# Performance work log

Measured on AMD Instinct MI355X. Metric: run time of the kernel, lower is better.

Reference implementation:

```python
import jax, jax.numpy as jnp
import numpy as np

N, C, H, W = 4, 64, 64, 64
K = 3


def _unfold(x, k):
    """torch F.unfold with padding k//2: [n,c,h,w] -> [n, c*k*k, h*w].
    Feature ordering matches torch: index = c*k*k + i*k + j."""
    p = k // 2
    n, c, h, w = x.shape
    xp = jnp.pad(x, ((0, 0), (0, 0), (p, p), (p, p)))
    patches = jnp.stack(
        [xp[:, :, i:i + h, j:j + w] for i in range(k) for j in range(k)], axis=2
    )  # [n, c, k*k, h, w]
    return patches.reshape(n, c * k * k, h * w)


def _mask_vec(c, k):
    # causal patch mask from __init__: zero out center-and-right of middle row and all rows below
    m = np.ones((c, k, k), np.float32)
    m[:, k // 2, k // 2:] = 0
    m[:, k // 2 + 1:, :] = 0
    return jnp.asarray(m.reshape(1, c * k * k, 1))


def setup_inputs() -> dict:
    key = jax.random.key(0)
    k1, k2 = jax.random.split(key)
    y_hat = jax.random.normal(k1, (N, C, H, W), dtype=jnp.float32)
    y_prob = jax.random.uniform(k2, (N, 1, H, W), dtype=jnp.float32)
    return {"y_hat": y_hat, "y_prob": y_prob}


def reference(y_hat, y_prob):
    k = K
    n, c, h, w = y_hat.shape
    L = h * w
    mask = _mask_vec(c, k)

    u = _unfold(y_hat, k) * mask                              # [n, c*k*k, L]
    u = u / jnp.maximum(jnp.linalg.norm(u, axis=1, keepdims=True), 1e-12)
    R = jnp.einsum('nfl,nfm->nlm', u, u)                      # [n, L, L] cosine sims

    # eval path: keep strictly-upper triangle (causal: l < m)
    row = jnp.arange(L)[:, None]
    col = jnp.arange(L)[None, :]
    R = jnp.where(col > row, R, 0.0)

    R_star = jnp.max(R, axis=1)                               # [n, L]
    arg = jnp.argmax(R, axis=1).astype(jnp.int32)             # [n, L]

    y_unf = _unfold(y_hat, k)                                 # [n, c*k*k, L]
    ref_unfold = jnp.take_along_axis(y_unf, arg[:, None, :], axis=2)

    prob_unf = y_prob.reshape(n, -1, L)                       # 1x1 unfold
    U_unf = jnp.take_along_axis(prob_unf, arg[:, None, :], axis=2)

    S = R_star.reshape(n, 1, h, w)
    U = U_unf.reshape(n, -1, h, w)

    # eval-mode position-0 overrides
    S = S.at[:, :, 0, 0].set(1e-8)
    U = U.at[:, :, 0, 0].set(1e-8)
    ref_unfold = ref_unfold.at[:, :, 0].set(0.0)
    arg = arg.at[:, 0].set(-1)

    S = jnp.clip(S, 1e-8, 1.0)
    U = jnp.clip(U, 1e-8, 1.0)
    return S, U, ref_unfold, arg
```

## Files before the change

### kernel.cpp

```cpp
#include <hip/hip_runtime.h>
#include <stdint.h>

#define Nn 4
#define Cc 64
#define LL 4096
#define KK 256
#define TRI2 528

typedef _Float16 half8 __attribute__((ext_vector_type(8)));
typedef float f32x16 __attribute__((ext_vector_type(16)));
typedef float f32x4 __attribute__((ext_vector_type(4)));
typedef unsigned short ushort8v __attribute__((ext_vector_type(8)));

__device__ __forceinline__ unsigned f2ord(float f) {
    unsigned u = __float_as_uint(f);
    return u ^ ((u & 0x80000000u) ? 0xFFFFFFFFu : 0x80000000u);
}
__device__ __forceinline__ float ord2f(unsigned o) {
    unsigned u = (o & 0x80000000u) ? (o ^ 0x80000000u) : ~o;
    return __uint_as_float(u);
}
__device__ __forceinline__ unsigned short h2u(_Float16 h) {
    union { _Float16 f; unsigned short u; } x; x.f = h; return x.u;
}

__global__ __launch_bounds__(256) void build_v(const float* __restrict__ yhat,
                                               unsigned short* __restrict__ VhT,
                                               unsigned short* __restrict__ VlT,
                                               float* __restrict__ yhatT,
                                               unsigned long long* __restrict__ best) {
    int blk = blockIdx.x;
    int xcd = blk & 7;
    int n = xcd >> 1;
    int i64 = (blk >> 3) + (xcd & 1) * 128;
    int tid = threadIdx.x;
    if (tid < 16) best[(size_t)n * LL + i64 * 16 + tid] = 0ull;

    int cg = tid & 15;
    int l = i64 * 16 + (tid >> 4);
    int y = l >> 6, x = l & 63;
    const float* src = yhat + (size_t)n * (Cc * LL);

    float vals[16];
    float ctr[4];
    float sumsq = 0.f;
#pragma unroll
    for (int ci = 0; ci < 4; ++ci) {
        const float* p = src + (cg * 4 + ci) * LL;
        float t0 = (y > 0 && x > 0)  ? p[l - 65] : 0.f;
        float t1 = (y > 0)           ? p[l - 64] : 0.f;
        float t2 = (y > 0 && x < 63) ? p[l - 63] : 0.f;
        float t3 = (x > 0)           ? p[l - 1]  : 0.f;
        ctr[ci] = p[l];
        vals[ci * 4 + 0] = t0; vals[ci * 4 + 1] = t1;
        vals[ci * 4 + 2] = t2; vals[ci * 4 + 3] = t3;
        sumsq += t0 * t0 + t1 * t1 + t2 * t2 + t3 * t3;
    }
    sumsq += __shfl_xor(sumsq, 1, 64);
    sumsq += __shfl_xor(sumsq, 2, 64);
    sumsq += __shfl_xor(sumsq, 4, 64);
    sumsq += __shfl_xor(sumsq, 8, 64);
    float inv = 1.f / fmaxf(sqrtf(sumsq), 1e-12f);

    f32x4 cv; cv.x = ctr[0]; cv.y = ctr[1]; cv.z = ctr[2]; cv.w = ctr[3];
    *(f32x4*)(yhatT + ((size_t)n * LL + l) * 64 + cg * 4) = cv;

    size_t pk = ((((size_t)n * 128 + (l >> 5)) * 16 + cg) << 9) + (l & 31) * 8;
    unsigned short* dh = VhT + pk;
    unsigned short* dl = VlT + pk;
    ushort8v hA, hB, lA, lB;
#pragma unroll
    for (int kk = 0; kk < 16; ++kk) {
        float v = vals[kk] * inv;
        _Float16 h = (fabsf(v) < 6.1035e-5f) ? (_Float16)0 : (_Float16)v;
        _Float16 lo = (_Float16)((v - (float)h) * 2048.0f);
        unsigned short hu = h2u(h * (_Float16)2048.0f);
        unsigned short lu = h2u(lo);
        if (kk < 8) { hA[kk] = hu; lA[kk] = lu; }
        else        { hB[kk - 8] = hu; lB[kk - 8] = lu; }
    }
    *(ushort8v*)(dh)       = hA;
    *(ushort8v*)(dh + 256) = hB;
    *(ushort8v*)(dl)       = lA;
    *(ushort8v*)(dl + 256) = lB;
}

__device__ __forceinline__ void loadset(const unsigned short* Ah0, const unsigned short* Ah1,
                                        const unsigned short* Al0, const unsigned short* Al1,
                                        const unsigned short* Bh0, const unsigned short* Bh1,
                                        const unsigned short* Bl0, const unsigned short* Bl1,
                                        int le,
                                        half8 (&al)[2][2], half8 (&ah)[2][2],
                                        half8 (&bl)[2][2], half8 (&bh)[2][2]) {
    al[0][0] = *(const half8*)(Al0 + le);       al[0][1] = *(const half8*)(Al0 + 512 + le);
    al[1][0] = *(const half8*)(Al1 + le);       al[1][1] = *(const half8*)(Al1 + 512 + le);
    bh[0][0] = *(const half8*)(Bh0 + le);       bh[0][1] = *(const half8*)(Bh0 + 512 + le);
    bh[1][0] = *(const half8*)(Bh1 + le);       bh[1][1] = *(const half8*)(Bh1 + 512 + le);
    ah[0][0] = *(const half8*)(Ah0 + le);       ah[0][1] = *(const half8*)(Ah0 + 512 + le);
    ah[1][0] = *(const half8*)(Ah1 + le);       ah[1][1] = *(const half8*)(Ah1 + 512 + le);
    bl[0][0] = *(const half8*)(Bl0 + le);       bl[0][1] = *(const half8*)(Bl0 + 512 + le);
    bl[1][0] = *(const half8*)(Bl1 + le);       bl[1][1] = *(const half8*)(Bl1 + 512 + le);
}

__device__ __forceinline__ void mfmaset(half8 (&al)[2][2], half8 (&ah)[2][2],
                                        half8 (&bl)[2][2], half8 (&bh)[2][2],
                                        f32x16 (&acc)[2][2]) {
    __builtin_amdgcn_s_setprio(1);
#pragma unroll
    for (int kc = 0; kc < 2; ++kc)
#pragma unroll
        for (int r = 0; r < 2; ++r)
#pragma unroll
            for (int c = 0; c < 2; ++c)
                acc[r][c] = __builtin_amdgcn_mfma_f32_32x32x16_f16(al[r][kc], bh[c][kc], acc[r][c], 0, 0, 0);
#pragma unroll
    for (int kc = 0; kc < 2; ++kc)
#pragma unroll
        for (int r = 0; r < 2; ++r)
#pragma unroll
            for (int c = 0; c < 2; ++c)
                acc[r][c] = __builtin_amdgcn_mfma_f32_32x32x16_f16(ah[r][kc], bl[c][kc], acc[r][c], 0, 0, 0);
#pragma unroll
    for (int kc = 0; kc < 2; ++kc)
#pragma unroll
        for (int r = 0; r < 2; ++r)
#pragma unroll
            for (int c = 0; c < 2; ++c)
                acc[r][c] = __builtin_amdgcn_mfma_f32_32x32x16_f16(ah[r][kc], bh[c][kc], acc[r][c], 0, 0, 0);
    __builtin_amdgcn_s_setprio(0);
}

__global__ __launch_bounds__(256) void simmax(const unsigned short* __restrict__ Vh,
                                              const unsigned short* __restrict__ Vl,
                                              unsigned long long* __restrict__ best) {
    int bx = blockIdx.x;
    int xcd = bx & 7, idx = bx >> 3;
    int n = xcd >> 1;
    int t = (xcd & 1) * 264 + idx;
    int j = (int)((sqrtf(8.f * (float)t + 1.f) - 1.f) * 0.5f);
    while ((j + 1) * (j + 2) / 2 <= t) ++j;
    while (j * (j + 1) / 2 > t) --j;
    int i = t - j * (j + 1) / 2;
    int l0 = i * 128, m0 = j * 128;

    int tid = threadIdx.x;
    int w = tid >> 6, lane = tid & 63;
    int r5 = lane & 31, h5 = lane >> 5;
    int rw = (w & 1) * 64;
    int cw = (w >> 1) * 64;
    if ((i == j) && (rw == 64) && (cw == 0)) return;

    const unsigned short* VhB = Vh + (size_t)n * (LL * KK);
    const unsigned short* VlB = Vl + (size_t)n * (LL * KK);

    int aRow = __builtin_amdgcn_readfirstlane((l0 + rw) >> 5);
    int bRow = __builtin_amdgcn_readfirstlane((m0 + cw) >> 5);
    const unsigned short* Ah0 = VhB + ((size_t)aRow << 13);
    const unsigned short* Ah1 = Ah0 + 8192;
    const unsigned short* Al0 = VlB + ((size_t)aRow << 13);
    const unsigned short* Al1 = Al0 + 8192;
    const unsigned short* Bh0 = VhB + ((size_t)bRow << 13);
    const unsigned short* Bh1 = Bh0 + 8192;
    const unsigned short* Bl0 = VlB + ((size_t)bRow << 13);
    const unsigned short* Bl1 = Bl0 + 8192;
    int le = lane * 8;

    f32x16 acc[2][2];
#pragma unroll
    for (int r = 0; r < 2; ++r)
#pragma unroll
        for (int c = 0; c < 2; ++c) acc[r][c] = (f32x16)0.f;

    half8 alA[2][2], ahA[2][2], blA[2][2], bhA[2][2];
    half8 alB[2][2], ahB[2][2], blB[2][2], bhB[2][2];

#define BUMP() do { Ah0 += 1024; Ah1 += 1024; Al0 += 1024; Al1 += 1024; \
                    Bh0 += 1024; Bh1 += 1024; Bl0 += 1024; Bl1 += 1024; } while (0)

    loadset(Ah0, Ah1, Al0, Al1, Bh0, Bh1, Bl0, Bl1, le, alA, ahA, blA, bhA);
    BUMP();
#pragma unroll 1
    for (int it = 0; it < 4; ++it) {
        loadset(Ah0, Ah1, Al0, Al1, Bh0, Bh1, Bl0, Bl1, le, alB, ahB, blB, bhB);
        BUMP();
        mfmaset(alA, ahA, blA, bhA, acc);
        if (it < 3) {
            loadset(Ah0, Ah1, Al0, Al1, Bh0, Bh1, Bl0, Bl1, le, alA, ahA, blA, bhA);
            BUMP();
        }
        mfmaset(alB, ahB, blB, bhB, acc);
    }
#undef BUMP

    unsigned long long* bb = best + (size_t)n * LL;
    const float s = 1.f / 4194304.f;
#pragma unroll
    for (int c = 0; c < 2; ++c) {
        int m = m0 + cw + c * 32 + r5;
        unsigned long long key = 0ull;
#pragma unroll
        for (int r = 0; r < 2; ++r)
#pragma unroll
            for (int g = 0; g < 16; ++g) {
                int l = l0 + rw + r * 32 + (g & 3) + 8 * (g >> 2) + 4 * h5;
                if (l < m) {
                    float v = acc[r][c][g] * s;
                    unsigned long long k2 =
                        ((unsigned long long)f2ord(v) << 32) |
                        (unsigned long long)(0xFFFFFFFFu - (unsigned)l);
                    key = (k2 > key) ? k2 : key;
                }
            }
        unsigned long long o = __shfl_xor(key, 32, 64);
        key = (o > key) ? o : key;
        if (h5 == 0 && key != 0ull) atomicMax(bb + m, key);
    }
}

__global__ __launch_bounds__(256) void writeout(const float* __restrict__ yhatT,
                                                const float* __restrict__ yprob,
                                                const unsigned long long* __restrict__ best,
                                                float* __restrict__ out) {
    __shared__ float P[576 * 17];

    int blk = blockIdx.x;
    int xcd = blk & 7;
    int n = xcd >> 1;
    int mb = (blk >> 3) + (xcd & 1) * 128;
    int m0 = mb * 16;
    int tid = threadIdx.x;
    int ml = tid >> 4;
    int cs = (tid & 15) * 4;
    int m = m0 + ml;

    unsigned long long key = best[(size_t)n * LL + m];
    unsigned l = 0xFFFFFFFFu - (unsigned)(key & 0xFFFFFFFFull);
    float val = ord2f((unsigned)(key >> 32));
    bool zero = (m == 0);
    if (zero) l = 0;
    int ly = (int)(l >> 6), lx = (int)(l & 63);

    float* Sout = out;
    float* Uout = out + 16384;
    float* Rout = out + 32768;
    float* Aout = out + 9469952;

    if (cs == 0) {
        float S = zero ? 1e-8f : fminf(fmaxf(val, 1e-8f), 1.0f);
        float U = zero ? 1e-8f : fminf(fmaxf(yprob[(size_t)n * LL + l], 1e-8f), 1.0f);
        Sout[(size_t)n * LL + m] = S;
        Uout[(size_t)n * LL + m] = U;
        Aout[(size_t)n * LL + m] = zero ? -1.0f : (float)l;
    }

    const float* T = yhatT + ((size_t)n * LL) * 64;
#pragma unroll
    for (int i = 0; i < 3; ++i) {
        int yy = ly + i - 1;
        bool rok = (!zero) && (yy >= 0) && (yy < 64);
#pragma unroll
        for (int jj = 0; jj < 3; ++jj) {
            int xx = lx + jj - 1;
            f32x4 v; v.x = 0.f; v.y = 0.f; v.z = 0.f; v.w = 0.f;
            if (rok && xx >= 0 && xx < 64)
                v = *(const f32x4*)(T + ((size_t)(yy * 64 + xx)) * 64 + cs);
            int ij = i * 3 + jj;
            P[((cs + 0) * 9 + ij) * 17 + ml] = v.x;
            P[((cs + 1) * 9 + ij) * 17 + ml] = v.y;
            P[((cs + 2) * 9 + ij) * 17 + ml] = v.z;
            P[((cs + 3) * 9 + ij) * 17 + ml] = v.w;
        }
    }
    __syncthreads();

    float* R = Rout + (size_t)n * (576 * LL) + m0;
    int fl = tid >> 4;
    int mm2 = tid & 15;
#pragma unroll 1
    for (int it2 = 0; it2 < 36; ++it2) {
        int f = it2 * 16 + fl;
        float v = P[f * 17 + mm2];
        __builtin_nontemporal_store(v, R + (size_t)f * LL + mm2);
    }
}

extern "C" void kernel_launch(void* const* d_in, const int* in_sizes, int n_in,
                              void* d_out, int out_size, void* d_ws, size_t ws_size,
                              hipStream_t stream) {
    const float* yhat  = (const float*)d_in[0];
    const float* yprob = (const float*)d_in[1];
    float* out = (float*)d_out;

    unsigned short* VhT = (unsigned short*)d_ws;
    unsigned short* VlT = (unsigned short*)((char*)d_ws + 8388608);
    unsigned long long* best =
        (unsigned long long*)((char*)d_ws + 16777216);
    float* yhatT = (float*)((char*)d_ws + 16908288);

    build_v<<<1024, 256, 0, stream>>>(yhat, VhT, VlT, yhatT, best);
    simmax<<<Nn * TRI2, 256, 0, stream>>>(VhT, VlT, best);
    writeout<<<1024, 256, 0, stream>>>(yhatT, yprob, best, out);
}
```

Measured before the change: 156.4 us.

## Stage A/B operand tiles in LDS via global_load_lds with double buffering

Replaces per-wave direct global loads of the hi/lo fp16 operands with a block-cooperative staging of the 128-row A and B tiles into a 64 KB shared buffer using global_load_lds, double-buffered across the 8 k-steps. Each wave then reads its fragments from LDS, so tiles shared between waves are fetched from global memory once per block instead of twice. The skipped diagonal wave now stays alive to take part in loads and barriers. The change adds a __syncthreads per k-step and heavy LDS use, which may cut occupancy.

Result: no change. 153.5 us (-1.8%).

```diff
diff --git a/kernel.cpp b/kernel.cpp
--- a/kernel.cpp
+++ b/kernel.cpp
@@ -85,23 +85,6 @@
     *(ushort8v*)(dl + 256) = lB;
 }
 
-__device__ __forceinline__ void loadset(const unsigned short* Ah0, const unsigned short* Ah1,
-                                        const unsigned short* Al0, const unsigned short* Al1,
-                                        const unsigned short* Bh0, const unsigned short* Bh1,
-                                        const unsigned short* Bl0, const unsigned short* Bl1,
-                                        int le,
-                                        half8 (&al)[2][2], half8 (&ah)[2][2],
-                                        half8 (&bl)[2][2], half8 (&bh)[2][2]) {
-    al[0][0] = *(const half8*)(Al0 + le);       al[0][1] = *(const half8*)(Al0 + 512 + le);
-    al[1][0] = *(const half8*)(Al1 + le);       al[1][1] = *(const half8*)(Al1 + 512 + le);
-    bh[0][0] = *(const half8*)(Bh0 + le);       bh[0][1] = *(const half8*)(Bh0 + 512 + le);
-    bh[1][0] = *(const half8*)(Bh1 + le);       bh[1][1] = *(const half8*)(Bh1 + 512 + le);
-    ah[0][0] = *(const half8*)(Ah0 + le);       ah[0][1] = *(const half8*)(Ah0 + 512 + le);
-    ah[1][0] = *(const half8*)(Ah1 + le);       ah[1][1] = *(const half8*)(Ah1 + 512 + le);
-    bl[0][0] = *(const half8*)(Bl0 + le);       bl[0][1] = *(const half8*)(Bl0 + 512 + le);
-    bl[1][0] = *(const half8*)(Bl1 + le);       bl[1][1] = *(const half8*)(Bl1 + 512 + le);
-}
-
 __device__ __forceinline__ void mfmaset(half8 (&al)[2][2], half8 (&ah)[2][2],
                                         half8 (&bl)[2][2], half8 (&bh)[2][2],
                                         f32x16 (&acc)[2][2]) {
@@ -133,6 +116,8 @@
 __global__ __launch_bounds__(256) void simmax(const unsigned short* __restrict__ Vh,
                                               const unsigned short* __restrict__ Vl,
                                               unsigned long long* __restrict__ best) {
+    __shared__ __align__(16) unsigned short S[32768];
+
     int bx = blockIdx.x;
     int xcd = bx & 7, idx = bx >> 3;
     int n = xcd >> 1;
@@ -148,22 +133,28 @@
     int r5 = lane & 31, h5 = lane >> 5;
     int rw = (w & 1) * 64;
     int cw = (w >> 1) * 64;
-    if ((i == j) && (rw == 64) && (cw == 0)) return;
+    bool skip = (i == j) && (rw == 64) && (cw == 0);
 
     const unsigned short* VhB = Vh + (size_t)n * (LL * KK);
     const unsigned short* VlB = Vl + (size_t)n * (LL * KK);
 
-    int aRow = __builtin_amdgcn_readfirstlane((l0 + rw) >> 5);
-    int bRow = __builtin_amdgcn_readfirstlane((m0 + cw) >> 5);
-    const unsigned short* Ah0 = VhB + ((size_t)aRow << 13);
-    const unsigned short* Ah1 = Ah0 + 8192;
-    const unsigned short* Al0 = VlB + ((size_t)aRow << 13);
-    const unsigned short* Al1 = Al0 + 8192;
-    const unsigned short* Bh0 = VhB + ((size_t)bRow << 13);
-    const unsigned short* Bh1 = Bh0 + 8192;
-    const unsigned short* Bl0 = VlB + ((size_t)bRow << 13);
-    const unsigned short* Bl1 = Bl0 + 8192;
-    int le = lane * 8;
+    int aRow0 = l0 >> 5;
+    int bRow0 = m0 >> 5;
+
+    const unsigned short* gsrc[8];
+    int lslot[8];
+#pragma unroll
+    for (int q = 0; q < 8; ++q) {
+        int c = w * 8 + q;
+        int side = c >> 4, rb = (c >> 2) & 3, lo = (c >> 1) & 1, kc = c & 1;
+        int rowblk = (side ? bRow0 : aRow0) + rb;
+        const unsigned short* base = lo ? VlB : VhB;
+        gsrc[q] = base + (((size_t)rowblk * 16 + kc) << 9) + lane * 8;
+        lslot[q] = c * 512;
+    }
+
+    int arb = (w & 1) * 2;
+    int brb = (w >> 1) * 2;
 
     f32x16 acc[2][2];
 #pragma unroll
@@ -171,27 +162,50 @@
 #pragma unroll
         for (int c = 0; c < 2; ++c) acc[r][c] = (f32x16)0.f;
 
-    half8 alA[2][2], ahA[2][2], blA[2][2], bhA[2][2];
-    half8 alB[2][2], ahB[2][2], blB[2][2], bhB[2][2];
-
-#define BUMP() do { Ah0 += 1024; Ah1 += 1024; Al0 += 1024; Al1 += 1024; \
-                    Bh0 += 1024; Bh1 += 1024; Bl0 += 1024; Bl1 += 1024; } while (0)
-
-    loadset(Ah0, Ah1, Al0, Al1, Bh0, Bh1, Bl0, Bl1, le, alA, ahA, blA, bhA);
-    BUMP();
-#pragma unroll 1
-    for (int it = 0; it < 4; ++it) {
-        loadset(Ah0, Ah1, Al0, Al1, Bh0, Bh1, Bl0, Bl1, le, alB, ahB, blB, bhB);
-        BUMP();
-        mfmaset(alA, ahA, blA, bhA, acc);
-        if (it < 3) {
-            loadset(Ah0, Ah1, Al0, Al1, Bh0, Bh1, Bl0, Bl1, le, alA, ahA, blA, bhA);
-            BUMP();
+#pragma unroll
+    for (int q = 0; q < 8; ++q)
+        __builtin_amdgcn_global_load_lds(
+            (const __attribute__((address_space(1))) void*)(gsrc[q]),
+            (__attribute__((address_space(3))) void*)(S + lslot[q]), 16, 0, 0);
+    __syncthreads();
+
+#pragma unroll
+    for (int kt = 0; kt < 8; ++kt) {
+        const int cur = (kt & 1) * 16384;
+        const int nxt = 16384 - cur;
+
+        if (kt < 7) {
+            const size_t kadv = (size_t)(kt + 1) * 1024;
+#pragma unroll
+            for (int q = 0; q < 8; ++q)
+                __builtin_amdgcn_global_load_lds(
+                    (const __attribute__((address_space(1))) void*)(gsrc[q] + kadv),
+                    (__attribute__((address_space(3))) void*)(S + nxt + lslot[q]), 16, 0, 0);
         }
-        mfmaset(alB, ahB, blB, bhB, acc);
-    }
-#undef BUMP
-
+
+        if (!skip) {
+            half8 al[2][2], ah[2][2], bl[2][2], bh[2][2];
+#pragma unroll
+            for (int kc = 0; kc < 2; ++kc)
+#pragma unroll
+                for (int r = 0; r < 2; ++r) {
+                    al[r][kc] = *(const half8*)(S + cur + ((arb + r) * 4 + 2 + kc) * 512 + lane * 8);
+                    bh[r][kc] = *(const half8*)(S + cur + (16 + (brb + r) * 4 + kc) * 512 + lane * 8);
+                }
+#pragma unroll
+            for (int kc = 0; kc < 2; ++kc)
+#pragma unroll
+                for (int r = 0; r < 2; ++r) {
+                    ah[r][kc] = *(const half8*)(S + cur + ((arb + r) * 4 + kc) * 512 + lane * 8);
+                    bl[r][kc] = *(const half8*)(S + cur + (16 + (brb + r) * 4 + 2 + kc) * 512 + lane * 8);
+                }
+            mfmaset(al, ah, bl, bh, acc);
+        }
+
+        if (kt < 7) __syncthreads();
+    }
+
+    if (skip) return;
     unsigned long long* bb = best + (size_t)n * LL;
     const float s = 1.f / 4194304.f;
 #pragma unroll
```
